# Kernel tuning notes

Hardware: AMD Instinct MI355X
Metric: run time of the kernel (lower is better)

Reference implementation:

```python
import jax, jax.numpy as jnp
import numpy as np

N_ITER = 3  # routing iterations (init kwarg n_iter)


def _squash_elemwise(s):
    # Original squash sums squares over dim=-1, but s_j has a trailing
    # singleton dim there, so it degenerates to an elementwise map:
    # s^2/(1+s^2) * s/|s| == s*|s|/(1+s^2).
    return s * jnp.abs(s) / (1.0 + s * s)


def setup_inputs() -> dict:
    key = jax.random.key(0)
    k1, k2 = jax.random.split(key)
    B, R, C, O, I = 256, 1152, 10, 16, 8
    x = jax.random.normal(k1, (B, R, I), dtype=jnp.float32)
    W = jax.random.normal(k2, (R, C, O, I), dtype=jnp.float32)  # nn.Parameter (leading 1 dropped)
    return {"x": x, "W": W}


def reference(x, W):
    # u_hat[b,r,c,o] = sum_i W[r,c,o,i] * x[b,r,i]
    u_hat = jnp.einsum('rcoi,bri->brco', W, x)  # [B,R,C,O]
    R, C = u_hat.shape[1], u_hat.shape[2]
    b = jnp.zeros((R, C), dtype=u_hat.dtype)  # routing logits, shared across batch
    v = None
    for it in range(N_ITER):
        c = jax.nn.softmax(b, axis=0)                     # softmax over routes (dim=1 orig)
        s = jnp.einsum('rc,brco->bco', c, u_hat)          # weighted sum over routes
        v = _squash_elemwise(s)                           # [B,C,O]
        if it < N_ITER - 1:
            # agreement, mean over batch (b_ij is [1,R,C,1] in original)
            b = b + jnp.einsum('brco,bco->brc', u_hat, v).mean(axis=0)
    return v[..., None]  # matches v_j.squeeze(1): [B, n_capsules, out_ch, 1]
```

## Files before the change

### kernel.cpp

```cpp
#include <hip/hip_runtime.h>
#include <math.h>

namespace {
constexpr int NB = 256;
constexpr int NR = 1152;
constexpr int NC = 10;
constexpr int NO = 16;
constexpr int NI = 8;
constexpr int K1 = NR * NI;
constexpr int NN = NC * NO;
constexpr int KS = 8;
constexpr int KC = K1 / KS;
constexpr int RPB = NR / KS;
}

using s16x8 = __attribute__((ext_vector_type(8))) short;
using f32x4 = __attribute__((ext_vector_type(4))) float;

__device__ __forceinline__ ushort f2bf(float f) {
    uint u = __float_as_uint(f);
    uint r = (u + 0x7FFFu + ((u >> 16) & 1u)) >> 16;
    return (ushort)r;
}

__device__ __forceinline__ s16x8 pack8(float4 a0, float4 a1) {
    s16x8 r;
    r[0] = (short)f2bf(a0.x); r[1] = (short)f2bf(a0.y);
    r[2] = (short)f2bf(a0.z); r[3] = (short)f2bf(a0.w);
    r[4] = (short)f2bf(a1.x); r[5] = (short)f2bf(a1.y);
    r[6] = (short)f2bf(a1.z); r[7] = (short)f2bf(a1.w);
    return r;
}

__device__ __forceinline__ s16x8 pack8s(float4 a0, float4 a1, float cr) {
    s16x8 r;
    r[0] = (short)f2bf(a0.x * cr); r[1] = (short)f2bf(a0.y * cr);
    r[2] = (short)f2bf(a0.z * cr); r[3] = (short)f2bf(a0.w * cr);
    r[4] = (short)f2bf(a1.x * cr); r[5] = (short)f2bf(a1.y * cr);
    r[6] = (short)f2bf(a1.z * cr); r[7] = (short)f2bf(a1.w * cr);
    return r;
}

template <bool FIRST>
__global__ __launch_bounds__(256) void k_a(const float* __restrict__ x,
                                           const float* __restrict__ W,
                                           const float* __restrict__ bbuf,
                                           float* __restrict__ spart,
                                           ushort* __restrict__ xTbf) {
    const int m0 = blockIdx.x * 16;
    const int c  = blockIdx.y;
    const int ks = blockIdx.z;
    const int tid = threadIdx.x;
    const int w = tid >> 6, l = tid & 63;

    __shared__ float red[4][16][16];
    __shared__ float crs[RPB];
    __shared__ float sred[4], sred2[4];

    if constexpr (FIRST) {
        __shared__ __align__(16) ushort T[32][264];
        const int bid = blockIdx.x + 16 * blockIdx.y + 160 * blockIdx.z;
        if (bid < K1 / 32) {
            const int k0 = bid * 32;
            #pragma unroll
            for (int j = 0; j < 8; ++j) {
                int f  = j * 256 + tid;
                int b  = f >> 3;
                int i4 = f & 7;
                float4 v = *reinterpret_cast<const float4*>(
                    x + (size_t)b * K1 + k0 + i4 * 4);
                T[i4 * 4 + 0][b] = f2bf(v.x);
                T[i4 * 4 + 1][b] = f2bf(v.y);
                T[i4 * 4 + 2][b] = f2bf(v.z);
                T[i4 * 4 + 3][b] = f2bf(v.w);
            }
            __syncthreads();
            #pragma unroll
            for (int j = 0; j < 4; ++j) {
                int g   = j * 256 + tid;
                int row = g >> 5;
                int q8  = g & 31;
                *reinterpret_cast<uint4*>(xTbf + (size_t)(k0 + row) * NB + q8 * 8) =
                    *reinterpret_cast<const uint4*>(&T[row][q8 * 8]);
            }
        }
    } else {
        float m = -1e30f;
        for (int r = tid; r < NR; r += 256) m = fmaxf(m, bbuf[r * NC + c]);
        #pragma unroll
        for (int off = 1; off < 64; off <<= 1) m = fmaxf(m, __shfl_xor(m, off));
        if (l == 0) sred[w] = m;
        __syncthreads();
        m = fmaxf(fmaxf(sred[0], sred[1]), fmaxf(sred[2], sred[3]));
        float s = 0.0f;
        for (int r = tid; r < NR; r += 256) s += expf(bbuf[r * NC + c] - m);
        #pragma unroll
        for (int off = 1; off < 64; off <<= 1) s += __shfl_xor(s, off);
        if (l == 0) sred2[w] = s;
        __syncthreads();
        s = sred2[0] + sred2[1] + sred2[2] + sred2[3];
        const float inv = 1.0f / s;
        for (int i = tid; i < RPB; i += 256)
            crs[i] = expf(bbuf[(ks * RPB + i) * NC + c] - m) * inv;
        __syncthreads();
    }

    const int kb = ks * KC + w * (KC / 4);
    const int lg = l >> 4;
    const float* ap = x + (size_t)(m0 + (l & 15)) * K1 + kb + 8 * lg;

    f32x4 acc = {0.f, 0.f, 0.f, 0.f};
    #pragma unroll
    for (int kk = 0; kk < KC / 4 / 32; ++kk) {
        const int k = kb + kk * 32 + 8 * lg;
        const int r = k >> 3;
        float4 a0 = *reinterpret_cast<const float4*>(ap + kk * 32);
        float4 a1 = *reinterpret_cast<const float4*>(ap + kk * 32 + 4);
        const float* wp = W + (((size_t)r * NC + c) * NO + (l & 15)) * NI;
        float4 b0 = *reinterpret_cast<const float4*>(wp);
        float4 b1 = *reinterpret_cast<const float4*>(wp + 4);
        const float cr = FIRST ? (1.0f / NR) : crs[r - ks * RPB];
        s16x8 a = pack8(a0, a1);
        s16x8 b = pack8s(b0, b1, cr);
        acc = __builtin_amdgcn_mfma_f32_16x16x32_bf16(a, b, acc, 0, 0, 0);
    }

    #pragma unroll
    for (int q = 0; q < 4; ++q) red[w][4 * lg + q][l & 15] = acc[q];
    __syncthreads();
    const int row = tid >> 4, col = tid & 15;
    float s2 = red[0][row][col] + red[1][row][col]
             + red[2][row][col] + red[3][row][col];
    spart[(size_t)ks * (NB * NN) + (size_t)(m0 + row) * NN + c * NO + col] = s2;
}

__global__ __launch_bounds__(256) void k_b(const ushort* __restrict__ xTbf,
                                           const float* __restrict__ spart,
                                           const float* __restrict__ W,
                                           float* __restrict__ bbuf,
                                           int it) {
    const int c = blockIdx.y;
    const int tid = threadIdx.x;
    const int w = tid >> 6, l = tid & 63;

    __shared__ __align__(16) ushort VT[16][264];

    for (int f = tid; f < NB * NO; f += 256) {
        int b  = f >> 4;
        int oo = f & 15;
        size_t idx = (size_t)b * NN + c * NO + oo;
        float s = 0.0f;
        #pragma unroll
        for (int ks = 0; ks < KS; ++ks) s += spart[(size_t)ks * NB * NN + idx];
        float v = s * fabsf(s) / (1.0f + s * s);
        VT[oo][b] = f2bf(v);
    }
    __syncthreads();

    #pragma unroll
    for (int t = 0; t < 4; ++t) {
        const int mt = blockIdx.x * 16 + w * 4 + t;
        const int m0 = mt * 16;
        const ushort* ap = xTbf + (size_t)(m0 + (l & 15)) * NB + 8 * (l >> 4);
        f32x4 acc = {0.f, 0.f, 0.f, 0.f};
        #pragma unroll
        for (int kk = 0; kk < NB / 32; ++kk) {
            s16x8 a = *reinterpret_cast<const s16x8*>(ap + kk * 32);
            s16x8 b = *reinterpret_cast<const s16x8*>(&VT[l & 15][32 * kk + 8 * (l >> 4)]);
            acc = __builtin_amdgcn_mfma_f32_16x16x32_bf16(a, b, acc, 0, 0, 0);
        }
        const int h  = l >> 4, o = l & 15;
        const int r  = (m0 >> 3) + (h >> 1);
        const int i0 = (4 * h) & 7;
        const float4 w4 = *reinterpret_cast<const float4*>(
            W + (((size_t)r * NC + c) * NO + o) * NI + i0);
        float s = acc[0] * w4.x + acc[1] * w4.y + acc[2] * w4.z + acc[3] * w4.w;
        s += __shfl_xor(s, 1);
        s += __shfl_xor(s, 2);
        s += __shfl_xor(s, 4);
        s += __shfl_xor(s, 8);
        s += __shfl_xor(s, 16);
        if (l == 0 || l == 32) {
            int rr = (m0 >> 3) + (l >> 5);
            float val = s * (1.0f / NB);
            if (it > 0) bbuf[(size_t)rr * NC + c] += val;
            else        bbuf[(size_t)rr * NC + c] = val;
        }
    }
}

__global__ __launch_bounds__(256) void k_bf(const float* __restrict__ spart,
                                            float* __restrict__ out) {
    const int m0 = blockIdx.x * 16;
    const int c  = blockIdx.y;
    const int row = threadIdx.x >> 4, col = threadIdx.x & 15;
    size_t idx = (size_t)(m0 + row) * NN + c * NO + col;
    float s = 0.0f;
    #pragma unroll
    for (int ks = 0; ks < KS; ++ks) s += spart[(size_t)ks * NB * NN + idx];
    out[idx] = s * fabsf(s) / (1.0f + s * s);
}

extern "C" void kernel_launch(void* const* d_in, const int* in_sizes, int n_in,
                              void* d_out, int out_size, void* d_ws, size_t ws_size,
                              hipStream_t stream) {
    const float* x = (const float*)d_in[0];
    const float* W = (const float*)d_in[1];
    float* out = (float*)d_out;

    float*  spart = (float*)d_ws;
    float*  bbuf  = spart + (size_t)KS * NB * NN;
    ushort* xTbf  = (ushort*)(bbuf + (size_t)NR * NC);

    dim3 ga(NB / 16, NC, KS);
    dim3 gb(36, NC);
    dim3 gf(NB / 16, NC);

    k_a<true><<<ga, 256, 0, stream>>>(x, W, nullptr, spart, xTbf);
    k_b<<<gb, 256, 0, stream>>>(xTbf, spart, W, bbuf, 0);
    k_a<false><<<ga, 256, 0, stream>>>(x, W, bbuf, spart, nullptr);
    k_b<<<gb, 256, 0, stream>>>(xTbf, spart, W, bbuf, 1);
    k_a<false><<<ga, 256, 0, stream>>>(x, W, bbuf, spart, nullptr);
    k_bf<<<gf, 256, 0, stream>>>(spart, out);
}
```

Before: 91.02 us.

## Drop split-K partials, fuse squash into routing GEMM, pre-convert inputs to bf16

Removes the 8-way split-K over routes. Each 512-thread block now reduces the full K dimension, and the squash is applied in the epilogue, so the spart partial buffer and the final k_bf kernel go away. The first pass also writes bf16 copies of W and x, which later passes read at half the bytes. v is written straight in transposed bf16 form for k_b, and b logits are ping-ponged between two buffers. The cost is a grid of only 160 blocks with a longer serial K loop per block, which lowers parallelism, plus extra conversion work in the first pass.

Measured after the change: 91.72 us. Within noise of the previous version (+0.8%).

```diff
diff --git a/kernel.cpp b/kernel.cpp
--- a/kernel.cpp
+++ b/kernel.cpp
@@ -9,9 +9,7 @@
 constexpr int NI = 8;
 constexpr int K1 = NR * NI;
 constexpr int NN = NC * NO;
-constexpr int KS = 8;
-constexpr int KC = K1 / KS;
-constexpr int RPB = NR / KS;
+constexpr int KW = K1 / 8;
 }
 
 using s16x8 = __attribute__((ext_vector_type(8))) short;
@@ -41,30 +39,46 @@
     return r;
 }
 
-template <bool FIRST>
-__global__ __launch_bounds__(256) void k_a(const float* __restrict__ x,
-                                           const float* __restrict__ W,
-                                           const float* __restrict__ bbuf,
-                                           float* __restrict__ spart,
-                                           ushort* __restrict__ xTbf) {
-    const int m0 = blockIdx.x * 16;
+__device__ __forceinline__ s16x8 scale8(uint4 u, float cr) {
+    s16x8 r;
+    r[0] = (short)f2bf(__uint_as_float((u.x & 0xFFFFu) << 16) * cr);
+    r[1] = (short)f2bf(__uint_as_float(u.x & 0xFFFF0000u) * cr);
+    r[2] = (short)f2bf(__uint_as_float((u.y & 0xFFFFu) << 16) * cr);
+    r[3] = (short)f2bf(__uint_as_float(u.y & 0xFFFF0000u) * cr);
+    r[4] = (short)f2bf(__uint_as_float((u.z & 0xFFFFu) << 16) * cr);
+    r[5] = (short)f2bf(__uint_as_float(u.z & 0xFFFF0000u) * cr);
+    r[6] = (short)f2bf(__uint_as_float((u.w & 0xFFFFu) << 16) * cr);
+    r[7] = (short)f2bf(__uint_as_float(u.w & 0xFFFF0000u) * cr);
+    return r;
+}
+
+template <int IT>
+__global__ __launch_bounds__(512) void k_af(const float* __restrict__ x,
+                                            const float* __restrict__ W,
+                                            ushort* __restrict__ Wb,
+                                            ushort* __restrict__ xbf,
+                                            ushort* __restrict__ xTbf,
+                                            const float* __restrict__ bb,
+                                            ushort* __restrict__ VT,
+                                            float* __restrict__ out) {
+    const int mt = blockIdx.x;
     const int c  = blockIdx.y;
-    const int ks = blockIdx.z;
+    const int m0 = mt * 16;
     const int tid = threadIdx.x;
     const int w = tid >> 6, l = tid & 63;
 
-    __shared__ float red[4][16][16];
-    __shared__ float crs[RPB];
-    __shared__ float sred[4], sred2[4];
-
-    if constexpr (FIRST) {
-        __shared__ __align__(16) ushort T[32][264];
-        const int bid = blockIdx.x + 16 * blockIdx.y + 160 * blockIdx.z;
-        if (bid < K1 / 32) {
-            const int k0 = bid * 32;
+    __shared__ __align__(16) ushort T[32][264];
+    __shared__ float red[8][16][16];
+    __shared__ float crs[NR];
+    __shared__ float sred[8], sred2[8];
+
+    if constexpr (IT == 0) {
+        const int bid = blockIdx.x + 16 * blockIdx.y;
+        for (int j = bid; j < K1 / 32; j += 160) {
+            const int k0 = j * 32;
             #pragma unroll
-            for (int j = 0; j < 8; ++j) {
-                int f  = j * 256 + tid;
+            for (int jj = 0; jj < 4; ++jj) {
+                int f  = jj * 512 + tid;
                 int b  = f >> 3;
                 int i4 = f & 7;
                 float4 v = *reinterpret_cast<const float4*>(
@@ -76,84 +90,116 @@
             }
             __syncthreads();
             #pragma unroll
-            for (int j = 0; j < 4; ++j) {
-                int g   = j * 256 + tid;
+            for (int jj = 0; jj < 2; ++jj) {
+                int g   = jj * 512 + tid;
                 int row = g >> 5;
                 int q8  = g & 31;
                 *reinterpret_cast<uint4*>(xTbf + (size_t)(k0 + row) * NB + q8 * 8) =
                     *reinterpret_cast<const uint4*>(&T[row][q8 * 8]);
             }
+            __syncthreads();
+        }
+        for (int e = bid * 512 + tid; e < NR * NC * NO; e += 160 * 512) {
+            const float* wp = W + (size_t)e * 8;
+            s16x8 p = pack8(*reinterpret_cast<const float4*>(wp),
+                            *reinterpret_cast<const float4*>(wp + 4));
+            *reinterpret_cast<uint4*>(Wb + (size_t)e * 8) =
+                *reinterpret_cast<uint4*>(&p);
+        }
+        for (int e = bid * 512 + tid; e < NB * (K1 / 8); e += 160 * 512) {
+            const float* xp = x + (size_t)e * 8;
+            s16x8 p = pack8(*reinterpret_cast<const float4*>(xp),
+                            *reinterpret_cast<const float4*>(xp + 4));
+            *reinterpret_cast<uint4*>(xbf + (size_t)e * 8) =
+                *reinterpret_cast<uint4*>(&p);
         }
     } else {
         float m = -1e30f;
-        for (int r = tid; r < NR; r += 256) m = fmaxf(m, bbuf[r * NC + c]);
+        for (int r = tid; r < NR; r += 512) m = fmaxf(m, bb[r * NC + c]);
         #pragma unroll
         for (int off = 1; off < 64; off <<= 1) m = fmaxf(m, __shfl_xor(m, off));
         if (l == 0) sred[w] = m;
         __syncthreads();
-        m = fmaxf(fmaxf(sred[0], sred[1]), fmaxf(sred[2], sred[3]));
+        m = sred[0];
+        #pragma unroll
+        for (int ww = 1; ww < 8; ++ww) m = fmaxf(m, sred[ww]);
         float s = 0.0f;
-        for (int r = tid; r < NR; r += 256) s += expf(bbuf[r * NC + c] - m);
+        for (int r = tid; r < NR; r += 512) s += expf(bb[r * NC + c] - m);
         #pragma unroll
         for (int off = 1; off < 64; off <<= 1) s += __shfl_xor(s, off);
         if (l == 0) sred2[w] = s;
         __syncthreads();
-        s = sred2[0] + sred2[1] + sred2[2] + sred2[3];
+        s = 0.0f;
+        #pragma unroll
+        for (int ww = 0; ww < 8; ++ww) s += sred2[ww];
         const float inv = 1.0f / s;
-        for (int i = tid; i < RPB; i += 256)
-            crs[i] = expf(bbuf[(ks * RPB + i) * NC + c] - m) * inv;
+        for (int r = tid; r < NR; r += 512)
+            crs[r] = expf(bb[r * NC + c] - m) * inv;
         __syncthreads();
     }
 
-    const int kb = ks * KC + w * (KC / 4);
+    const int kb = w * KW;
     const int lg = l >> 4;
-    const float* ap = x + (size_t)(m0 + (l & 15)) * K1 + kb + 8 * lg;
-
     f32x4 acc = {0.f, 0.f, 0.f, 0.f};
-    #pragma unroll
-    for (int kk = 0; kk < KC / 4 / 32; ++kk) {
-        const int k = kb + kk * 32 + 8 * lg;
-        const int r = k >> 3;
-        float4 a0 = *reinterpret_cast<const float4*>(ap + kk * 32);
-        float4 a1 = *reinterpret_cast<const float4*>(ap + kk * 32 + 4);
-        const float* wp = W + (((size_t)r * NC + c) * NO + (l & 15)) * NI;
-        float4 b0 = *reinterpret_cast<const float4*>(wp);
-        float4 b1 = *reinterpret_cast<const float4*>(wp + 4);
-        const float cr = FIRST ? (1.0f / NR) : crs[r - ks * RPB];
-        s16x8 a = pack8(a0, a1);
-        s16x8 b = pack8s(b0, b1, cr);
-        acc = __builtin_amdgcn_mfma_f32_16x16x32_bf16(a, b, acc, 0, 0, 0);
-    }
-
+
+    if constexpr (IT == 0) {
+        const float* ap = x + (size_t)(m0 + (l & 15)) * K1 + kb + 8 * lg;
+        #pragma unroll 4
+        for (int kk = 0; kk < KW / 32; ++kk) {
+            float4 a0 = *reinterpret_cast<const float4*>(ap + kk * 32);
+            float4 a1 = *reinterpret_cast<const float4*>(ap + kk * 32 + 4);
+            s16x8 a = pack8s(a0, a1, 1.0f / NR);
+            const int r = w * 144 + kk * 4 + lg;
+            const float* wp = W + ((size_t)r * NC + c) * 128 + (l & 15) * 8;
+            s16x8 b = pack8(*reinterpret_cast<const float4*>(wp),
+                            *reinterpret_cast<const float4*>(wp + 4));
+            acc = __builtin_amdgcn_mfma_f32_16x16x32_bf16(a, b, acc, 0, 0, 0);
+        }
+    } else {
+        const ushort* ap = xbf + (size_t)(m0 + (l & 15)) * K1 + kb + 8 * lg;
+        #pragma unroll 4
+        for (int kk = 0; kk < KW / 32; ++kk) {
+            uint4 ar = *reinterpret_cast<const uint4*>(ap + kk * 32);
+            const int r = w * 144 + kk * 4 + lg;
+            s16x8 a = scale8(ar, crs[r]);
+            s16x8 b = *reinterpret_cast<const s16x8*>(
+                Wb + ((size_t)r * NC + c) * 128 + (l & 15) * 8);
+            acc = __builtin_amdgcn_mfma_f32_16x16x32_bf16(a, b, acc, 0, 0, 0);
+        }
+    }
+
+    __syncthreads();
     #pragma unroll
     for (int q = 0; q < 4; ++q) red[w][4 * lg + q][l & 15] = acc[q];
     __syncthreads();
-    const int row = tid >> 4, col = tid & 15;
-    float s2 = red[0][row][col] + red[1][row][col]
-             + red[2][row][col] + red[3][row][col];
-    spart[(size_t)ks * (NB * NN) + (size_t)(m0 + row) * NN + c * NO + col] = s2;
+    if (tid < 256) {
+        const int row = tid >> 4, col = tid & 15;
+        float s = 0.0f;
+        #pragma unroll
+        for (int ww = 0; ww < 8; ++ww) s += red[ww][row][col];
+        float v = s * fabsf(s) / (1.0f + s * s);
+        if constexpr (IT == 2)
+            out[(size_t)(m0 + row) * NN + c * NO + col] = v;
+        else
+            VT[(size_t)(c * NO + col) * NB + m0 + row] = f2bf(v);
+    }
 }
 
 __global__ __launch_bounds__(256) void k_b(const ushort* __restrict__ xTbf,
-                                           const float* __restrict__ spart,
+                                           const ushort* __restrict__ VT,
                                            const float* __restrict__ W,
-                                           float* __restrict__ bbuf,
-                                           int it) {
+                                           const float* __restrict__ bbR,
+                                           float* __restrict__ bbW) {
     const int c = blockIdx.y;
     const int tid = threadIdx.x;
     const int w = tid >> 6, l = tid & 63;
 
-    __shared__ __align__(16) ushort VT[16][264];
-
-    for (int f = tid; f < NB * NO; f += 256) {
-        int b  = f >> 4;
-        int oo = f & 15;
-        size_t idx = (size_t)b * NN + c * NO + oo;
-        float s = 0.0f;
-        #pragma unroll
-        for (int ks = 0; ks < KS; ++ks) s += spart[(size_t)ks * NB * NN + idx];
-        float v = s * fabsf(s) / (1.0f + s * s);
-        VT[oo][b] = f2bf(v);
+    __shared__ __align__(16) ushort VTs[16][264];
+
+    for (int e = tid; e < 16 * 32; e += 256) {
+        int row = e >> 5, q8 = e & 31;
+        *reinterpret_cast<uint4*>(&VTs[row][q8 * 8]) =
+            *reinterpret_cast<const uint4*>(VT + (size_t)(c * NO + row) * NB + q8 * 8);
     }
     __syncthreads();
 
@@ -166,7 +212,8 @@
         #pragma unroll
         for (int kk = 0; kk < NB / 32; ++kk) {
             s16x8 a = *reinterpret_cast<const s16x8*>(ap + kk * 32);
-            s16x8 b = *reinterpret_cast<const s16x8*>(&VT[l & 15][32 * kk + 8 * (l >> 4)]);
+            s16x8 b = *reinterpret_cast<const s16x8*>(
+                &VTs[l & 15][32 * kk + 8 * (l >> 4)]);
             acc = __builtin_amdgcn_mfma_f32_16x16x32_bf16(a, b, acc, 0, 0, 0);
         }
         const int h  = l >> 4, o = l & 15;
@@ -183,22 +230,10 @@
         if (l == 0 || l == 32) {
             int rr = (m0 >> 3) + (l >> 5);
             float val = s * (1.0f / NB);
-            if (it > 0) bbuf[(size_t)rr * NC + c] += val;
-            else        bbuf[(size_t)rr * NC + c] = val;
-        }
-    }
-}
-
-__global__ __launch_bounds__(256) void k_bf(const float* __restrict__ spart,
-                                            float* __restrict__ out) {
-    const int m0 = blockIdx.x * 16;
-    const int c  = blockIdx.y;
-    const int row = threadIdx.x >> 4, col = threadIdx.x & 15;
-    size_t idx = (size_t)(m0 + row) * NN + c * NO + col;
-    float s = 0.0f;
-    #pragma unroll
-    for (int ks = 0; ks < KS; ++ks) s += spart[(size_t)ks * NB * NN + idx];
-    out[idx] = s * fabsf(s) / (1.0f + s * s);
+            bbW[(size_t)rr * NC + c] =
+                (bbR ? bbR[(size_t)rr * NC + c] : 0.0f) + val;
+        }
+    }
 }
 
 extern "C" void kernel_launch(void* const* d_in, const int* in_sizes, int n_in,
@@ -208,18 +243,19 @@
     const float* W = (const float*)d_in[1];
     float* out = (float*)d_out;
 
-    float*  spart = (float*)d_ws;
-    float*  bbuf  = spart + (size_t)KS * NB * NN;
-    ushort* xTbf  = (ushort*)(bbuf + (size_t)NR * NC);
-
-    dim3 ga(NB / 16, NC, KS);
+    ushort* xTbf = (ushort*)d_ws;
+    ushort* Wb   = xTbf + (size_t)K1 * NB;
+    ushort* xbf  = Wb + (size_t)NR * NC * NO * NI;
+    ushort* VT   = xbf + (size_t)NB * K1;
+    float*  bbuf0 = (float*)(VT + (size_t)NN * NB);
+    float*  bbuf1 = bbuf0 + (size_t)NR * NC;
+
+    dim3 ga(NB / 16, NC);
     dim3 gb(36, NC);
-    dim3 gf(NB / 16, NC);
-
-    k_a<true><<<ga, 256, 0, stream>>>(x, W, nullptr, spart, xTbf);
-    k_b<<<gb, 256, 0, stream>>>(xTbf, spart, W, bbuf, 0);
-    k_a<false><<<ga, 256, 0, stream>>>(x, W, bbuf, spart, nullptr);
-    k_b<<<gb, 256, 0, stream>>>(xTbf, spart, W, bbuf, 1);
-    k_a<false><<<ga, 256, 0, stream>>>(x, W, bbuf, spart, nullptr);
-    k_bf<<<gf, 256, 0, stream>>>(spart, out);
-}
+
+    k_af<0><<<ga, 512, 0, stream>>>(x, W, Wb, xbf, xTbf, nullptr, VT, nullptr);
+    k_b<<<gb, 256, 0, stream>>>(xTbf, VT, W, nullptr, bbuf0);
+    k_af<1><<<ga, 512, 0, stream>>>(x, W, Wb, xbf, xTbf, bbuf0, VT, nullptr);
+    k_b<<<gb, 256, 0, stream>>>(xTbf, VT, W, bbuf0, bbuf1);
+    k_af<2><<<ga, 512, 0, stream>>>(x, W, Wb, xbf, xTbf, bbuf1, nullptr, out);
+}
```
